# Optimization experiments

Measured on AMD Instinct MI355X. Metric: run time of the kernel, lower is better.

## Reference

```python
import jax, jax.numpy as jnp
import numpy as np
from math import sqrt

B, LQ, LKV = 4, 1024, 1024
QD = KD = VD = 1024
MODEL_DIM = 1024
H = 16
HD = MODEL_DIM // H  # per-head model_dim = 64


def setup_inputs() -> dict:
    key = jax.random.key(0)
    ks = jax.random.split(key, 10)
    s = 0.02
    return {
        "queries": jax.random.normal(ks[0], (B, LQ, QD), jnp.float32),
        "context": jax.random.normal(ks[1], (B, LKV, KD), jnp.float32),
        # stacked per-head linear weights (torch Linear: y = x @ W.T + b); store as [H, in, out]
        "Wq": jax.random.normal(ks[2], (H, QD, HD), jnp.float32) * s,
        "bq": jax.random.normal(ks[3], (H, HD), jnp.float32) * s,
        "Wk": jax.random.normal(ks[4], (KD, HD * 1 * H), jnp.float32).reshape(H, KD, HD) * s,
        "bk": jax.random.normal(ks[5], (H, HD), jnp.float32) * s,
        "Wv": jax.random.normal(ks[6], (H, VD, HD), jnp.float32) * s,
        "bv": jax.random.normal(ks[7], (H, HD), jnp.float32) * s,
        "Wo": jax.random.normal(ks[8], (H * HD, MODEL_DIM), jnp.float32) * s,
        "bo": jax.random.normal(ks[9], (MODEL_DIM,), jnp.float32) * s,
    }


def reference(queries, context, Wq, bq, Wk, bk, Wv, bv, Wo, bo):
    # queries: [B,Lq,Dq]; context: [B,Lkv,Dk]
    # Per-head projections, batched over heads (equivalent to the torch per-head loop).
    q = jnp.einsum("bld,hdm->bhlm", queries, Wq) + bq[None, :, None, :]  # [B,H,Lq,hd]
    k = jnp.einsum("bld,hdm->bhlm", context, Wk) + bk[None, :, None, :]  # [B,H,Lkv,hd]
    v = jnp.einsum("bld,hdm->bhlm", context, Wv) + bv[None, :, None, :]  # [B,H,Lkv,hd]

    scale = 1.0 / sqrt(HD)
    scores = jnp.einsum("bhqd,bhkd->bhqk", q, k) * scale  # [B,H,Lq,Lkv]
    att = jax.nn.softmax(scores, axis=-1)
    head_out = jnp.einsum("bhqk,bhkd->bhqd", att, v)  # [B,H,Lq,hd]

    # torch concatenates heads along the last dim in head order 0..H-1
    multi = head_out.transpose(0, 2, 1, 3).reshape(B, LQ, H * HD)
    residual = q.transpose(0, 2, 1, 3).reshape(B, LQ, H * HD)

    out = multi @ Wo + bo  # [B,Lq,model_dim]
    return out, residual
```

## Files before the change

kernel.cpp:

```cpp
#include <hip/hip_runtime.h>
#include <hip/hip_bf16.h>


typedef unsigned short u16;
typedef __attribute__((ext_vector_type(8))) short short8;
typedef __attribute__((ext_vector_type(4))) float f32x4;

__device__ __forceinline__ float bf2f(u16 u) {
    union { unsigned int i; float f; } c;
    c.i = ((unsigned int)u) << 16;
    return c.f;
}

__device__ __forceinline__ u16 f2bf(float f) {
    unsigned int x = __float_as_uint(f);
    unsigned int r = (x + 0x7fffu + ((x >> 16) & 1u)) >> 16;
    return (u16)r;
}

__device__ __forceinline__ void glds16(u16* lds, const u16* g) {
    __builtin_amdgcn_global_load_lds(
        (const __attribute__((address_space(1))) void*)g,
        (__attribute__((address_space(3))) void*)lds, 16, 0, 0);
}

__global__ __launch_bounds__(256) void prep(
    const float* __restrict__ q, const float* __restrict__ ctx,
    const float* __restrict__ Wq, const float* __restrict__ Wk,
    const float* __restrict__ Wv, const float* __restrict__ Wo,
    u16* __restrict__ Aq, u16* __restrict__ Ac,
    u16* __restrict__ Wqt, u16* __restrict__ Wkt,
    u16* __restrict__ Wvt, u16* __restrict__ Wot)
{
    __shared__ float ls[64][65];
    const int t = threadIdx.x;
    int bid = blockIdx.x;

    if (bid < 4096) {
        const float* in = (bid < 2048) ? q : ctx;
        u16* out = (bid < 2048) ? Aq : Ac;
        size_t i = ((size_t)(bid & 2047) * 256 + t) * 8;
        float4 v0 = *(const float4*)(in + i);
        float4 v1 = *(const float4*)(in + i + 4);
        short8 p;
        p[0] = (short)f2bf(v0.x); p[1] = (short)f2bf(v0.y);
        p[2] = (short)f2bf(v0.z); p[3] = (short)f2bf(v0.w);
        p[4] = (short)f2bf(v1.x); p[5] = (short)f2bf(v1.y);
        p[6] = (short)f2bf(v1.z); p[7] = (short)f2bf(v1.w);
        *(short8*)(out + i) = p;
        return;
    }
    bid -= 4096;
    const float* in; u16* out; int C; size_t moff; int rt, ct;
    if (bid < 768) {
        const int m = bid >> 8, idx = bid & 255;
        in = (m == 0) ? Wq : (m == 1) ? Wk : Wv;
        out = (m == 0) ? Wqt : (m == 1) ? Wkt : Wvt;
        C = 64; rt = (idx & 15) * 64; ct = 0; moff = (size_t)(idx >> 4) * 65536;
    } else {
        const int idx = bid - 768;
        in = Wo; out = Wot; C = 1024; moff = 0;
        rt = (idx & 15) * 64; ct = (idx >> 4) * 64;
    }
    #pragma unroll
    for (int i = 0; i < 4; ++i) {
        int s = i * 256 + t;
        int row = s >> 4, chunk = s & 15;
        float4 v = *(const float4*)(in + moff + (size_t)(rt + row) * C + ct + chunk * 4);
        ls[row][chunk * 4 + 0] = v.x;
        ls[row][chunk * 4 + 1] = v.y;
        ls[row][chunk * 4 + 2] = v.z;
        ls[row][chunk * 4 + 3] = v.w;
    }
    __syncthreads();
    #pragma unroll
    for (int i = 0; i < 2; ++i) {
        int s = i * 256 + t;
        int n = s >> 3, kc = s & 7;
        short8 p;
        #pragma unroll
        for (int j = 0; j < 8; ++j) p[j] = (short)f2bf(ls[kc * 8 + j][n]);
        *(short8*)(out + moff + (size_t)(ct + n) * 1024 + rt + kc * 8) = p;
    }
}

__device__ __forceinline__ void gemm_core(
    const u16* __restrict__ A, const u16* __restrict__ Wt,
    int m0, u16* As, u16* Bs, f32x4 (&acc)[4][4])
{
    const int t = threadIdx.x;
    const int w = t >> 6, lane = t & 63;
    const int quad = lane >> 4, c = lane & 15;
    const int srow = w * 32 + (lane >> 2);
    const int sch = lane & 3;

    const u16* gA = A + (size_t)(m0 + srow) * 1024 + sch * 8;
    const u16* gB = Wt + (size_t)srow * 1024 + sch * 8;
    u16* lA = As + w * 32 * 32;
    u16* lB = Bs + w * 32 * 32;
    const u16* afr = As + ((w >> 1) * 64 + c) * 32 + quad * 8;
    const u16* bfr = Bs + ((w & 1) * 64 + c) * 32 + quad * 8;

    for (int kt = 0; kt < 1024; kt += 32) {
        glds16(lA,           gA + kt);
        glds16(lA + 16 * 32, gA + kt + 16 * 1024);
        glds16(lB,           gB + kt);
        glds16(lB + 16 * 32, gB + kt + 16 * 1024);
        __syncthreads();
        short8 af[4], bf[4];
        #pragma unroll
        for (int rs = 0; rs < 4; ++rs) af[rs] = *(const short8*)(afr + rs * 16 * 32);
        #pragma unroll
        for (int cs = 0; cs < 4; ++cs) bf[cs] = *(const short8*)(bfr + cs * 16 * 32);
        #pragma unroll
        for (int rs = 0; rs < 4; ++rs)
            #pragma unroll
            for (int cs = 0; cs < 4; ++cs)
                acc[rs][cs] = __builtin_amdgcn_mfma_f32_16x16x32_bf16(
                    af[rs], bf[cs], acc[rs][cs], 0, 0, 0);
        __syncthreads();
    }
}

__global__ __launch_bounds__(256, 3) void gemm_qkv(
    const u16* __restrict__ Aq, const u16* __restrict__ Ac,
    const u16* __restrict__ Wqt, const u16* __restrict__ Wkt,
    const u16* __restrict__ Wvt,
    const float* __restrict__ bq, const float* __restrict__ bk,
    const float* __restrict__ bv,
    u16* __restrict__ qws, u16* __restrict__ kws, u16* __restrict__ vtws,
    float* __restrict__ resid)
{
    __shared__ u16 As[128 * 32];
    __shared__ u16 Bs[128 * 32];
    const int n0 = blockIdx.x * 128, m0 = blockIdx.y * 128, z = blockIdx.z;
    const int t = threadIdx.x;
    const int w = t >> 6, lane = t & 63;
    const int quad = lane >> 4, c = lane & 15;

    const u16* A = (z == 0) ? Aq : Ac;
    const u16* Wt = ((z == 0) ? Wqt : (z == 1) ? Wkt : Wvt) + (size_t)n0 * 1024;
    const float* bias = (z == 0) ? bq : (z == 1) ? bk : bv;

    f32x4 acc[4][4] = {};
    gemm_core(A, Wt, m0, As, Bs, acc);

    const int h = blockIdx.x * 2 + (w & 1);
    float bb[4];
    #pragma unroll
    for (int cs = 0; cs < 4; ++cs) bb[cs] = bias[h * 64 + cs * 16 + c];

    if (z == 2) {
        #pragma unroll
        for (int rs = 0; rs < 4; ++rs) {
            const int l0 = m0 + (w >> 1) * 64 + rs * 16 + quad * 4;
            const int b = l0 >> 10, l = l0 & 1023;
            #pragma unroll
            for (int cs = 0; cs < 4; ++cs) {
                const int hd = cs * 16 + c;
                ushort4 pk;
                pk.x = f2bf(acc[rs][cs][0] + bb[cs]);
                pk.y = f2bf(acc[rs][cs][1] + bb[cs]);
                pk.z = f2bf(acc[rs][cs][2] + bb[cs]);
                pk.w = f2bf(acc[rs][cs][3] + bb[cs]);
                *(ushort4*)(vtws + ((size_t)(b * 16 + h) * 64 + hd) * 1024 + l) = pk;
            }
        }
    } else {
        u16* dst = (z == 0) ? qws : kws;
        const float scale = (z == 0) ? 0.125f : 1.0f;
        #pragma unroll
        for (int rs = 0; rs < 4; ++rs) {
            #pragma unroll
            for (int r = 0; r < 4; ++r) {
                const int row = m0 + (w >> 1) * 64 + rs * 16 + quad * 4 + r;
                const int b = row >> 10, l = row & 1023;
                u16* drow = dst + (((size_t)(b * 16 + h) * 1024) + l) * 64;
                float* rrow = (z == 0) ? (resid + (size_t)row * 1024 + h * 64) : nullptr;
                #pragma unroll
                for (int cs = 0; cs < 4; ++cs) {
                    float v = acc[rs][cs][r] + bb[cs];
                    drow[cs * 16 + c] = f2bf(v * scale);
                    if (z == 0) rrow[cs * 16 + c] = v;
                }
            }
        }
    }
}

__global__ __launch_bounds__(256, 3) void gemm_out(
    const u16* __restrict__ A, const u16* __restrict__ Wot,
    const float* __restrict__ bo, float* __restrict__ out)
{
    __shared__ u16 As[128 * 32];
    __shared__ u16 Bs[64 * 32];
    const int f = blockIdx.x;
    const int xcd = f & 7, k = f >> 3;
    const int m0 = (xcd * 4 + (k & 3)) * 128;
    const int n0 = (k >> 2) * 64;
    const int t = threadIdx.x;
    const int w = t >> 6, lane = t & 63;
    const int quad = lane >> 4, c = lane & 15;

    const int arow = w * 32 + (lane >> 2), ach = lane & 3;
    const int brow = w * 16 + (lane >> 2);
    const u16* gA = A + (size_t)(m0 + arow) * 1024 + ach * 8;
    const u16* gB = Wot + (size_t)(n0 + brow) * 1024 + ach * 8;
    u16* lA = As + w * 32 * 32;
    u16* lB = Bs + w * 16 * 32;
    const u16* afr = As + ((w >> 1) * 64 + c) * 32 + quad * 8;
    const u16* bfr = Bs + ((w & 1) * 32 + c) * 32 + quad * 8;

    f32x4 acc[4][2] = {};
    for (int kt = 0; kt < 1024; kt += 32) {
        glds16(lA,           gA + kt);
        glds16(lA + 16 * 32, gA + kt + 16 * 1024);
        glds16(lB,           gB + kt);
        __syncthreads();
        short8 af[4], bf[2];
        #pragma unroll
        for (int rs = 0; rs < 4; ++rs) af[rs] = *(const short8*)(afr + rs * 16 * 32);
        #pragma unroll
        for (int cs = 0; cs < 2; ++cs) bf[cs] = *(const short8*)(bfr + cs * 16 * 32);
        #pragma unroll
        for (int rs = 0; rs < 4; ++rs)
            #pragma unroll
            for (int cs = 0; cs < 2; ++cs)
                acc[rs][cs] = __builtin_amdgcn_mfma_f32_16x16x32_bf16(
                    af[rs], bf[cs], acc[rs][cs], 0, 0, 0);
        __syncthreads();
    }

    const int nb = n0 + (w & 1) * 32;
    float bb[2];
    #pragma unroll
    for (int cs = 0; cs < 2; ++cs) bb[cs] = bo[nb + cs * 16 + c];

    #pragma unroll
    for (int rs = 0; rs < 4; ++rs) {
        #pragma unroll
        for (int r = 0; r < 4; ++r) {
            const int row = m0 + (w >> 1) * 64 + rs * 16 + quad * 4 + r;
            float* orow = out + (size_t)row * 1024 + nb;
            #pragma unroll
            for (int cs = 0; cs < 2; ++cs)
                orow[cs * 16 + c] = acc[rs][cs][r] + bb[cs];
        }
    }
}

__global__ __launch_bounds__(256, 4) void attn_mfma(
    const u16* __restrict__ qws, const u16* __restrict__ kws,
    const u16* __restrict__ vtws, u16* __restrict__ multi)
{
    __shared__ u16 Ks[64 * 64];
    __shared__ u16 Vs[64 * 64];
    const int t = threadIdx.x;
    const int wave = t >> 6, lane = t & 63;
    const int quad = lane >> 4, c = lane & 15;
    const int bh = blockIdx.y, b = bh >> 4, h = bh & 15;
    const int q0 = blockIdx.x * 64 + wave * 16;

    const u16* qb = qws + ((size_t)bh * 1024 + q0) * 64;
    const u16* kb = kws + (size_t)bh * 65536;
    const u16* vb = vtws + (size_t)bh * 65536;

    short8 qa0 = *(const short8*)(qb + (size_t)c * 64 + quad * 8);
    short8 qa1 = *(const short8*)(qb + (size_t)c * 64 + 32 + quad * 8);

    const int srow = wave * 16 + (lane >> 3);
    const int gch = (lane & 7) ^ ((lane >> 3) & 7);
    u16* ldsK0 = Ks + (wave * 16) * 64;
    u16* ldsK1 = Ks + (wave * 16 + 8) * 64;
    u16* ldsV0 = Vs + (wave * 16) * 64;
    u16* ldsV1 = Vs + (wave * 16 + 8) * 64;
    const u16* gK0 = kb + (size_t)srow * 64 + gch * 8;
    const u16* gK1 = kb + (size_t)(srow + 8) * 64 + gch * 8;
    const u16* gV0 = vb + (size_t)srow * 1024 + gch * 8;
    const u16* gV1 = vb + (size_t)(srow + 8) * 1024 + gch * 8;

    f32x4 O[4] = {};
    float lsum = 0.f;
    const int cx = c & 7;

    for (int kt = 0; kt < 1024; kt += 64) {
        glds16(ldsK0, gK0 + (size_t)kt * 64);
        glds16(ldsK1, gK1 + (size_t)kt * 64);
        glds16(ldsV0, gV0 + kt);
        glds16(ldsV1, gV1 + kt);
        __syncthreads();

        #pragma unroll
        for (int hb = 0; hb < 2; ++hb) {
            const int kbase = hb * 32;
            const u16* kr0 = Ks + (kbase + c) * 64;
            const u16* kr1 = Ks + (kbase + 16 + c) * 64;
            short8 kf00 = *(const short8*)(kr0 + (quad ^ cx) * 8);
            short8 kf01 = *(const short8*)(kr0 + ((4 + quad) ^ cx) * 8);
            short8 kf10 = *(const short8*)(kr1 + (quad ^ cx) * 8);
            short8 kf11 = *(const short8*)(kr1 + ((4 + quad) ^ cx) * 8);

            f32x4 st0 = {}, st1 = {};
            st0 = __builtin_amdgcn_mfma_f32_16x16x32_bf16(kf00, qa0, st0, 0, 0, 0);
            st0 = __builtin_amdgcn_mfma_f32_16x16x32_bf16(kf01, qa1, st0, 0, 0, 0);
            st1 = __builtin_amdgcn_mfma_f32_16x16x32_bf16(kf10, qa0, st1, 0, 0, 0);
            st1 = __builtin_amdgcn_mfma_f32_16x16x32_bf16(kf11, qa1, st1, 0, 0, 0);

            f32x4 p0, p1;
            #pragma unroll
            for (int r = 0; r < 4; ++r) {
                p0[r] = __expf(st0[r]);
                p1[r] = __expf(st1[r]);
                lsum += p0[r] + p1[r];
            }

            short8 pa;
            #pragma unroll
            for (int j = 0; j < 8; ++j) {
                const int srcl = ((2 * quad + (j >> 2)) & 3) * 16 + c;
                float v0 = __shfl(p0[j & 3], srcl);
                float v1 = __shfl(p1[j & 3], srcl);
                float v = (quad < 2) ? v0 : v1;
                pa[j] = (short)(__float_as_uint(v) >> 16);
            }

            #pragma unroll
            for (int nt = 0; nt < 4; ++nt) {
                const u16* vr = Vs + (nt * 16 + c) * 64;
                short8 vf = *(const short8*)(vr + ((hb * 4 + quad) ^ cx) * 8);
                O[nt] = __builtin_amdgcn_mfma_f32_16x16x32_bf16(pa, vf, O[nt], 0, 0, 0);
            }
        }
        __syncthreads();
    }

    lsum += __shfl_xor(lsum, 16);
    lsum += __shfl_xor(lsum, 32);
    float inv[4];
    #pragma unroll
    for (int r = 0; r < 4; ++r) inv[r] = 1.0f / __shfl(lsum, quad * 4 + r);

    u16* ob = multi + ((size_t)b * 1024 + q0 + quad * 4) * 1024 + h * 64 + c;
    #pragma unroll
    for (int r = 0; r < 4; ++r) {
        u16* orow = ob + (size_t)r * 1024;
        orow[0]  = f2bf(O[0][r] * inv[r]);
        orow[16] = f2bf(O[1][r] * inv[r]);
        orow[32] = f2bf(O[2][r] * inv[r]);
        orow[48] = f2bf(O[3][r] * inv[r]);
    }
}

extern "C" void kernel_launch(void* const* d_in, const int* in_sizes, int n_in,
                              void* d_out, int out_size, void* d_ws, size_t ws_size,
                              hipStream_t stream) {
    const float* queries = (const float*)d_in[0];
    const float* context = (const float*)d_in[1];
    const float* Wq = (const float*)d_in[2];
    const float* bq = (const float*)d_in[3];
    const float* Wk = (const float*)d_in[4];
    const float* bk = (const float*)d_in[5];
    const float* Wv = (const float*)d_in[6];
    const float* bv = (const float*)d_in[7];
    const float* Wo = (const float*)d_in[8];
    const float* bo = (const float*)d_in[9];

    float* out = (float*)d_out;
    float* resid = out + (size_t)4 * 1024 * 1024;

    const size_t M1 = 1024 * 1024;
    u16* Aq   = (u16*)d_ws;
    u16* Ac   = Aq + 4 * M1;
    u16* Wqt  = Ac + 4 * M1;
    u16* Wkt  = Wqt + M1;
    u16* Wvt  = Wkt + M1;
    u16* Wot  = Wvt + M1;
    u16* qws  = Wot + M1;
    u16* kws  = qws + 4 * M1;
    u16* vtws = kws + 4 * M1;
    u16* mws  = vtws + 4 * M1;

    prep<<<5120, 256, 0, stream>>>(queries, context, Wq, Wk, Wv, Wo,
                                   Aq, Ac, Wqt, Wkt, Wvt, Wot);
    gemm_qkv<<<dim3(8, 32, 3), 256, 0, stream>>>(Aq, Ac, Wqt, Wkt, Wvt,
                                                 bq, bk, bv, qws, kws, vtws, resid);
    attn_mfma<<<dim3(16, 64), 256, 0, stream>>>(qws, kws, vtws, mws);
    gemm_out<<<512, 256, 0, stream>>>(mws, Wot, bo, out);
}
```

Before: 212.0 us.

## Fuse K and V projections sharing context tiles; route attention P through LDS

The QKV projection kernel now computes K and V in the same block, so each context tile is loaded into LDS once and multiplied against both weight tiles. This halves context-tile traffic for the K/V GEMMs but doubles accumulator registers, lowers the occupancy bound to 2 and leaves z=0 blocks doing half the work of z=1 blocks (load imbalance). The attention kernel switches from shuffle-based transposition of P to writing P as bf16 into a per-wave padded LDS buffer and reading it back as the A operand. Row sums are reduced with xor-shuffles across the 16 columns.

```diff
diff --git a/kernel.cpp b/kernel.cpp
--- a/kernel.cpp
+++ b/kernel.cpp
@@ -84,45 +84,7 @@
     }
 }
 
-__device__ __forceinline__ void gemm_core(
-    const u16* __restrict__ A, const u16* __restrict__ Wt,
-    int m0, u16* As, u16* Bs, f32x4 (&acc)[4][4])
-{
-    const int t = threadIdx.x;
-    const int w = t >> 6, lane = t & 63;
-    const int quad = lane >> 4, c = lane & 15;
-    const int srow = w * 32 + (lane >> 2);
-    const int sch = lane & 3;
-
-    const u16* gA = A + (size_t)(m0 + srow) * 1024 + sch * 8;
-    const u16* gB = Wt + (size_t)srow * 1024 + sch * 8;
-    u16* lA = As + w * 32 * 32;
-    u16* lB = Bs + w * 32 * 32;
-    const u16* afr = As + ((w >> 1) * 64 + c) * 32 + quad * 8;
-    const u16* bfr = Bs + ((w & 1) * 64 + c) * 32 + quad * 8;
-
-    for (int kt = 0; kt < 1024; kt += 32) {
-        glds16(lA,           gA + kt);
-        glds16(lA + 16 * 32, gA + kt + 16 * 1024);
-        glds16(lB,           gB + kt);
-        glds16(lB + 16 * 32, gB + kt + 16 * 1024);
-        __syncthreads();
-        short8 af[4], bf[4];
-        #pragma unroll
-        for (int rs = 0; rs < 4; ++rs) af[rs] = *(const short8*)(afr + rs * 16 * 32);
-        #pragma unroll
-        for (int cs = 0; cs < 4; ++cs) bf[cs] = *(const short8*)(bfr + cs * 16 * 32);
-        #pragma unroll
-        for (int rs = 0; rs < 4; ++rs)
-            #pragma unroll
-            for (int cs = 0; cs < 4; ++cs)
-                acc[rs][cs] = __builtin_amdgcn_mfma_f32_16x16x32_bf16(
-                    af[rs], bf[cs], acc[rs][cs], 0, 0, 0);
-        __syncthreads();
-    }
-}
-
-__global__ __launch_bounds__(256, 3) void gemm_qkv(
+__global__ __launch_bounds__(256, 2) void gemm_qkv(
     const u16* __restrict__ Aq, const u16* __restrict__ Ac,
     const u16* __restrict__ Wqt, const u16* __restrict__ Wkt,
     const u16* __restrict__ Wvt,
@@ -132,57 +94,125 @@
     float* __restrict__ resid)
 {
     __shared__ u16 As[128 * 32];
-    __shared__ u16 Bs[128 * 32];
+    __shared__ u16 B1[128 * 32];
+    __shared__ u16 B2[128 * 32];
     const int n0 = blockIdx.x * 128, m0 = blockIdx.y * 128, z = blockIdx.z;
     const int t = threadIdx.x;
     const int w = t >> 6, lane = t & 63;
     const int quad = lane >> 4, c = lane & 15;
-
-    const u16* A = (z == 0) ? Aq : Ac;
-    const u16* Wt = ((z == 0) ? Wqt : (z == 1) ? Wkt : Wvt) + (size_t)n0 * 1024;
-    const float* bias = (z == 0) ? bq : (z == 1) ? bk : bv;
-
-    f32x4 acc[4][4] = {};
-    gemm_core(A, Wt, m0, As, Bs, acc);
-
+    const int srow = w * 32 + (lane >> 2);
+    const int sch = lane & 3;
+
+    u16* lA = As + w * 32 * 32;
+    u16* lB1 = B1 + w * 32 * 32;
+    u16* lB2 = B2 + w * 32 * 32;
+    const u16* afr = As + ((w >> 1) * 64 + c) * 32 + quad * 8;
+    const u16* b1fr = B1 + ((w & 1) * 64 + c) * 32 + quad * 8;
+    const u16* b2fr = B2 + ((w & 1) * 64 + c) * 32 + quad * 8;
     const int h = blockIdx.x * 2 + (w & 1);
-    float bb[4];
-    #pragma unroll
-    for (int cs = 0; cs < 4; ++cs) bb[cs] = bias[h * 64 + cs * 16 + c];
-
-    if (z == 2) {
+
+    if (z == 0) {
+        const u16* gA = Aq + (size_t)(m0 + srow) * 1024 + sch * 8;
+        const u16* gB = Wqt + (size_t)(n0 + srow) * 1024 + sch * 8;
+        f32x4 acc[4][4] = {};
+        for (int kt = 0; kt < 1024; kt += 32) {
+            glds16(lA,           gA + kt);
+            glds16(lA + 16 * 32, gA + kt + 16 * 1024);
+            glds16(lB1,           gB + kt);
+            glds16(lB1 + 16 * 32, gB + kt + 16 * 1024);
+            __syncthreads();
+            short8 af[4], bf[4];
+            #pragma unroll
+            for (int rs = 0; rs < 4; ++rs) af[rs] = *(const short8*)(afr + rs * 16 * 32);
+            #pragma unroll
+            for (int cs = 0; cs < 4; ++cs) bf[cs] = *(const short8*)(b1fr + cs * 16 * 32);
+            #pragma unroll
+            for (int rs = 0; rs < 4; ++rs)
+                #pragma unroll
+                for (int cs = 0; cs < 4; ++cs)
+                    acc[rs][cs] = __builtin_amdgcn_mfma_f32_16x16x32_bf16(
+                        af[rs], bf[cs], acc[rs][cs], 0, 0, 0);
+            __syncthreads();
+        }
+        float bb[4];
+        #pragma unroll
+        for (int cs = 0; cs < 4; ++cs) bb[cs] = bq[h * 64 + cs * 16 + c];
+        #pragma unroll
+        for (int rs = 0; rs < 4; ++rs)
+            #pragma unroll
+            for (int r = 0; r < 4; ++r) {
+                const int row = m0 + (w >> 1) * 64 + rs * 16 + quad * 4 + r;
+                const int b = row >> 10, l = row & 1023;
+                u16* drow = qws + (((size_t)(b * 16 + h) * 1024) + l) * 64;
+                float* rrow = resid + (size_t)row * 1024 + h * 64;
+                #pragma unroll
+                for (int cs = 0; cs < 4; ++cs) {
+                    float v = acc[rs][cs][r] + bb[cs];
+                    drow[cs * 16 + c] = f2bf(v * 0.125f);
+                    rrow[cs * 16 + c] = v;
+                }
+            }
+    } else {
+        const u16* gA = Ac + (size_t)(m0 + srow) * 1024 + sch * 8;
+        const u16* gBk = Wkt + (size_t)(n0 + srow) * 1024 + sch * 8;
+        const u16* gBv = Wvt + (size_t)(n0 + srow) * 1024 + sch * 8;
+        f32x4 acck[4][4] = {};
+        f32x4 accv[4][4] = {};
+        for (int kt = 0; kt < 1024; kt += 32) {
+            glds16(lA,            gA + kt);
+            glds16(lA + 16 * 32,  gA + kt + 16 * 1024);
+            glds16(lB1,           gBk + kt);
+            glds16(lB1 + 16 * 32, gBk + kt + 16 * 1024);
+            glds16(lB2,           gBv + kt);
+            glds16(lB2 + 16 * 32, gBv + kt + 16 * 1024);
+            __syncthreads();
+            short8 af[4], bkf[4], bvf[4];
+            #pragma unroll
+            for (int rs = 0; rs < 4; ++rs) af[rs] = *(const short8*)(afr + rs * 16 * 32);
+            #pragma unroll
+            for (int cs = 0; cs < 4; ++cs) {
+                bkf[cs] = *(const short8*)(b1fr + cs * 16 * 32);
+                bvf[cs] = *(const short8*)(b2fr + cs * 16 * 32);
+            }
+            #pragma unroll
+            for (int rs = 0; rs < 4; ++rs)
+                #pragma unroll
+                for (int cs = 0; cs < 4; ++cs) {
+                    acck[rs][cs] = __builtin_amdgcn_mfma_f32_16x16x32_bf16(
+                        af[rs], bkf[cs], acck[rs][cs], 0, 0, 0);
+                    accv[rs][cs] = __builtin_amdgcn_mfma_f32_16x16x32_bf16(
+                        af[rs], bvf[cs], accv[rs][cs], 0, 0, 0);
+                }
+            __syncthreads();
+        }
+        float bbk[4], bbv[4];
+        #pragma unroll
+        for (int cs = 0; cs < 4; ++cs) {
+            bbk[cs] = bk[h * 64 + cs * 16 + c];
+            bbv[cs] = bv[h * 64 + cs * 16 + c];
+        }
         #pragma unroll
         for (int rs = 0; rs < 4; ++rs) {
+            #pragma unroll
+            for (int r = 0; r < 4; ++r) {
+                const int row = m0 + (w >> 1) * 64 + rs * 16 + quad * 4 + r;
+                const int b = row >> 10, l = row & 1023;
+                u16* drow = kws + (((size_t)(b * 16 + h) * 1024) + l) * 64;
+                #pragma unroll
+                for (int cs = 0; cs < 4; ++cs)
+                    drow[cs * 16 + c] = f2bf(acck[rs][cs][r] + bbk[cs]);
+            }
             const int l0 = m0 + (w >> 1) * 64 + rs * 16 + quad * 4;
             const int b = l0 >> 10, l = l0 & 1023;
             #pragma unroll
             for (int cs = 0; cs < 4; ++cs) {
                 const int hd = cs * 16 + c;
                 ushort4 pk;
-                pk.x = f2bf(acc[rs][cs][0] + bb[cs]);
-                pk.y = f2bf(acc[rs][cs][1] + bb[cs]);
-                pk.z = f2bf(acc[rs][cs][2] + bb[cs]);
-                pk.w = f2bf(acc[rs][cs][3] + bb[cs]);
+                pk.x = f2bf(accv[rs][cs][0] + bbv[cs]);
+                pk.y = f2bf(accv[rs][cs][1] + bbv[cs]);
+                pk.z = f2bf(accv[rs][cs][2] + bbv[cs]);
+                pk.w = f2bf(accv[rs][cs][3] + bbv[cs]);
                 *(ushort4*)(vtws + ((size_t)(b * 16 + h) * 64 + hd) * 1024 + l) = pk;
-            }
-        }
-    } else {
-        u16* dst = (z == 0) ? qws : kws;
-        const float scale = (z == 0) ? 0.125f : 1.0f;
-        #pragma unroll
-        for (int rs = 0; rs < 4; ++rs) {
-            #pragma unroll
-            for (int r = 0; r < 4; ++r) {
-                const int row = m0 + (w >> 1) * 64 + rs * 16 + quad * 4 + r;
-                const int b = row >> 10, l = row & 1023;
-                u16* drow = dst + (((size_t)(b * 16 + h) * 1024) + l) * 64;
-                float* rrow = (z == 0) ? (resid + (size_t)row * 1024 + h * 64) : nullptr;
-                #pragma unroll
-                for (int cs = 0; cs < 4; ++cs) {
-                    float v = acc[rs][cs][r] + bb[cs];
-                    drow[cs * 16 + c] = f2bf(v * scale);
-                    if (z == 0) rrow[cs * 16 + c] = v;
-                }
             }
         }
     }
@@ -255,6 +285,7 @@
 {
     __shared__ u16 Ks[64 * 64];
     __shared__ u16 Vs[64 * 64];
+    __shared__ u16 Ps[4][16 * 72];
     const int t = threadIdx.x;
     const int wave = t >> 6, lane = t & 63;
     const int quad = lane >> 4, c = lane & 15;
@@ -280,7 +311,8 @@
     const u16* gV1 = vb + (size_t)(srow + 8) * 1024 + gch * 8;
 
     f32x4 O[4] = {};
-    float lsum = 0.f;
+    float ps[4] = {0.f, 0.f, 0.f, 0.f};
+    u16* pw = &Ps[wave][0];
     const int cx = c & 7;
 
     for (int kt = 0; kt < 1024; kt += 64) {
@@ -290,55 +322,50 @@
         glds16(ldsV1, gV1 + kt);
         __syncthreads();
 
-        #pragma unroll
-        for (int hb = 0; hb < 2; ++hb) {
-            const int kbase = hb * 32;
-            const u16* kr0 = Ks + (kbase + c) * 64;
-            const u16* kr1 = Ks + (kbase + 16 + c) * 64;
-            short8 kf00 = *(const short8*)(kr0 + (quad ^ cx) * 8);
-            short8 kf01 = *(const short8*)(kr0 + ((4 + quad) ^ cx) * 8);
-            short8 kf10 = *(const short8*)(kr1 + (quad ^ cx) * 8);
-            short8 kf11 = *(const short8*)(kr1 + ((4 + quad) ^ cx) * 8);
-
-            f32x4 st0 = {}, st1 = {};
-            st0 = __builtin_amdgcn_mfma_f32_16x16x32_bf16(kf00, qa0, st0, 0, 0, 0);
-            st0 = __builtin_amdgcn_mfma_f32_16x16x32_bf16(kf01, qa1, st0, 0, 0, 0);
-            st1 = __builtin_amdgcn_mfma_f32_16x16x32_bf16(kf10, qa0, st1, 0, 0, 0);
-            st1 = __builtin_amdgcn_mfma_f32_16x16x32_bf16(kf11, qa1, st1, 0, 0, 0);
-
-            f32x4 p0, p1;
+        f32x4 s[4];
+        #pragma unroll
+        for (int nt = 0; nt < 4; ++nt) {
+            const u16* kr = Ks + (nt * 16 + c) * 64;
+            short8 kb0 = *(const short8*)(kr + ((quad ^ cx)) * 8);
+            short8 kb1 = *(const short8*)(kr + (((4 + quad) ^ cx)) * 8);
+            f32x4 z = {};
+            z = __builtin_amdgcn_mfma_f32_16x16x32_bf16(qa0, kb0, z, 0, 0, 0);
+            z = __builtin_amdgcn_mfma_f32_16x16x32_bf16(qa1, kb1, z, 0, 0, 0);
+            s[nt] = z;
+        }
+
+        #pragma unroll
+        for (int nt = 0; nt < 4; ++nt)
             #pragma unroll
             for (int r = 0; r < 4; ++r) {
-                p0[r] = __expf(st0[r]);
-                p1[r] = __expf(st1[r]);
-                lsum += p0[r] + p1[r];
+                float p = __expf(s[nt][r]);
+                ps[r] += p;
+                pw[(quad * 4 + r) * 72 + nt * 16 + c] = (u16)(__float_as_uint(p) >> 16);
             }
-
-            short8 pa;
-            #pragma unroll
-            for (int j = 0; j < 8; ++j) {
-                const int srcl = ((2 * quad + (j >> 2)) & 3) * 16 + c;
-                float v0 = __shfl(p0[j & 3], srcl);
-                float v1 = __shfl(p1[j & 3], srcl);
-                float v = (quad < 2) ? v0 : v1;
-                pa[j] = (short)(__float_as_uint(v) >> 16);
-            }
-
-            #pragma unroll
-            for (int nt = 0; nt < 4; ++nt) {
-                const u16* vr = Vs + (nt * 16 + c) * 64;
-                short8 vf = *(const short8*)(vr + ((hb * 4 + quad) ^ cx) * 8);
-                O[nt] = __builtin_amdgcn_mfma_f32_16x16x32_bf16(pa, vf, O[nt], 0, 0, 0);
-            }
+        short8 pa0 = *(const short8*)(pw + c * 72 + quad * 8);
+        short8 pa1 = *(const short8*)(pw + c * 72 + 32 + quad * 8);
+
+        #pragma unroll
+        for (int nt = 0; nt < 4; ++nt) {
+            const u16* vr = Vs + (nt * 16 + c) * 64;
+            short8 vb0 = *(const short8*)(vr + ((quad ^ cx)) * 8);
+            short8 vb1 = *(const short8*)(vr + (((4 + quad) ^ cx)) * 8);
+            O[nt] = __builtin_amdgcn_mfma_f32_16x16x32_bf16(pa0, vb0, O[nt], 0, 0, 0);
+            O[nt] = __builtin_amdgcn_mfma_f32_16x16x32_bf16(pa1, vb1, O[nt], 0, 0, 0);
         }
         __syncthreads();
     }
 
-    lsum += __shfl_xor(lsum, 16);
-    lsum += __shfl_xor(lsum, 32);
     float inv[4];
     #pragma unroll
-    for (int r = 0; r < 4; ++r) inv[r] = 1.0f / __shfl(lsum, quad * 4 + r);
+    for (int r = 0; r < 4; ++r) {
+        float sum = ps[r];
+        sum += __shfl_xor(sum, 1);
+        sum += __shfl_xor(sum, 2);
+        sum += __shfl_xor(sum, 4);
+        sum += __shfl_xor(sum, 8);
+        inv[r] = 1.0f / sum;
+    }
 
     u16* ob = multi + ((size_t)b * 1024 + q0 + quad * 4) * 1024 + h * 64 + c;
     #pragma unroll
@@ -382,7 +409,7 @@
 
     prep<<<5120, 256, 0, stream>>>(queries, context, Wq, Wk, Wv, Wo,
                                    Aq, Ac, Wqt, Wkt, Wvt, Wot);
-    gemm_qkv<<<dim3(8, 32, 3), 256, 0, stream>>>(Aq, Ac, Wqt, Wkt, Wvt,
+    gemm_qkv<<<dim3(8, 32, 2), 256, 0, stream>>>(Aq, Ac, Wqt, Wkt, Wvt,
                                                  bq, bk, bv, qws, kws, vtws, resid);
     attn_mfma<<<dim3(16, 64), 256, 0, stream>>>(qws, kws, vtws, mws);
     gemm_out<<<512, 256, 0, stream>>>(mws, Wot, bo, out);
```

Result: faster. 202.1 us (-4.7%).

## Split attention KV range across waves with cross-wave reduction and XCD-aware block mapping

Applied to the files above, without the earlier changes.

Restructures the attention kernel so every wave processes all 64 queries of the block over its own quarter of the KV sequence, staging K/V per wave without block barriers, then reduces partial outputs and row sums across waves through LDS. Probabilities go through per-wave LDS instead of lane shuffles, and blocks are remapped so each XCD handles a contiguous set of batch-heads for L2 reuse. The aim is to remove per-tile __syncthreads and shuffle overhead and to raise MFMA reuse of each K/V fragment. In exchange it uses more LDS and registers (occupancy hint lowered to 2), and partial outputs are rounded to bf16 before the cross-wave sum, which adds rounding error.

```diff
diff --git a/kernel.cpp b/kernel.cpp
--- a/kernel.cpp
+++ b/kernel.cpp
@@ -3,18 +3,19 @@
 
 
 typedef unsigned short u16;
+typedef unsigned int u32;
 typedef __attribute__((ext_vector_type(8))) short short8;
 typedef __attribute__((ext_vector_type(4))) float f32x4;
 
 __device__ __forceinline__ float bf2f(u16 u) {
-    union { unsigned int i; float f; } c;
-    c.i = ((unsigned int)u) << 16;
-    return c.f;
+    union { u32 i; float f; } cv;
+    cv.i = ((u32)u) << 16;
+    return cv.f;
 }
 
 __device__ __forceinline__ u16 f2bf(float f) {
-    unsigned int x = __float_as_uint(f);
-    unsigned int r = (x + 0x7fffu + ((x >> 16) & 1u)) >> 16;
+    u32 x = __float_as_uint(f);
+    u32 r = (x + 0x7fffu + ((x >> 16) & 1u)) >> 16;
     return (u16)r;
 }
 
@@ -249,105 +250,163 @@
     }
 }
 
-__global__ __launch_bounds__(256, 4) void attn_mfma(
+__global__ __launch_bounds__(256, 2) void attn_mfma(
     const u16* __restrict__ qws, const u16* __restrict__ kws,
     const u16* __restrict__ vtws, u16* __restrict__ multi)
 {
-    __shared__ u16 Ks[64 * 64];
-    __shared__ u16 Vs[64 * 64];
+    __shared__ u16 smem[26112];
     const int t = threadIdx.x;
-    const int wave = t >> 6, lane = t & 63;
+    const int w = t >> 6, lane = t & 63;
     const int quad = lane >> 4, c = lane & 15;
-    const int bh = blockIdx.y, b = bh >> 4, h = bh & 15;
-    const int q0 = blockIdx.x * 64 + wave * 16;
+    const int f = blockIdx.x;
+    const int xcd = f & 7, j = f >> 3;
+    const int bh = xcd * 8 + (j & 7);
+    const int qt = j >> 3;
+    const int b = bh >> 4, h = bh & 15;
+    const int q0 = qt * 64;
 
     const u16* qb = qws + ((size_t)bh * 1024 + q0) * 64;
     const u16* kb = kws + (size_t)bh * 65536;
     const u16* vb = vtws + (size_t)bh * 65536;
 
-    short8 qa0 = *(const short8*)(qb + (size_t)c * 64 + quad * 8);
-    short8 qa1 = *(const short8*)(qb + (size_t)c * 64 + 32 + quad * 8);
-
-    const int srow = wave * 16 + (lane >> 3);
-    const int gch = (lane & 7) ^ ((lane >> 3) & 7);
-    u16* ldsK0 = Ks + (wave * 16) * 64;
-    u16* ldsK1 = Ks + (wave * 16 + 8) * 64;
-    u16* ldsV0 = Vs + (wave * 16) * 64;
-    u16* ldsV1 = Vs + (wave * 16 + 8) * 64;
-    const u16* gK0 = kb + (size_t)srow * 64 + gch * 8;
-    const u16* gK1 = kb + (size_t)(srow + 8) * 64 + gch * 8;
-    const u16* gV0 = vb + (size_t)srow * 1024 + gch * 8;
-    const u16* gV1 = vb + (size_t)(srow + 8) * 1024 + gch * 8;
-
-    f32x4 O[4] = {};
-    float lsum = 0.f;
+    short8 qa[4][2];
+    #pragma unroll
+    for (int mt = 0; mt < 4; ++mt) {
+        const u16* qr = qb + (size_t)(mt * 16 + c) * 64 + quad * 8;
+        qa[mt][0] = *(const short8*)(qr);
+        qa[mt][1] = *(const short8*)(qr + 32);
+    }
+
+    u16* stgK = smem + w * 4096;
+    u16* stgV = stgK + 2048;
+    u16* pw   = smem + 16384 + w * 2304;
+    float* lsumLDS = (float*)(smem + 25600);
+
+    const int gkc = (lane & 7) ^ ((lane >> 3) & 7);
+    const int gvc = (lane & 3) ^ ((lane >> 3) & 3);
+    const int krow = lane >> 3;
+    const int vdim = lane >> 2;
+
+    f32x4 O[4][4] = {};
+    f32x4 lp[4] = {};
+    const int kw = w * 256;
     const int cx = c & 7;
-
-    for (int kt = 0; kt < 1024; kt += 64) {
-        glds16(ldsK0, gK0 + (size_t)kt * 64);
-        glds16(ldsK1, gK1 + (size_t)kt * 64);
-        glds16(ldsV0, gV0 + kt);
-        glds16(ldsV1, gV1 + kt);
-        __syncthreads();
-
-        #pragma unroll
-        for (int hb = 0; hb < 2; ++hb) {
-            const int kbase = hb * 32;
-            const u16* kr0 = Ks + (kbase + c) * 64;
-            const u16* kr1 = Ks + (kbase + 16 + c) * 64;
-            short8 kf00 = *(const short8*)(kr0 + (quad ^ cx) * 8);
-            short8 kf01 = *(const short8*)(kr0 + ((4 + quad) ^ cx) * 8);
-            short8 kf10 = *(const short8*)(kr1 + (quad ^ cx) * 8);
-            short8 kf11 = *(const short8*)(kr1 + ((4 + quad) ^ cx) * 8);
-
-            f32x4 st0 = {}, st1 = {};
-            st0 = __builtin_amdgcn_mfma_f32_16x16x32_bf16(kf00, qa0, st0, 0, 0, 0);
-            st0 = __builtin_amdgcn_mfma_f32_16x16x32_bf16(kf01, qa1, st0, 0, 0, 0);
-            st1 = __builtin_amdgcn_mfma_f32_16x16x32_bf16(kf10, qa0, st1, 0, 0, 0);
-            st1 = __builtin_amdgcn_mfma_f32_16x16x32_bf16(kf11, qa1, st1, 0, 0, 0);
-
-            f32x4 p0, p1;
+    const int vsw = quad ^ ((c >> 1) & 3);
+
+    for (int i = 0; i < 8; ++i) {
+        const int kt = kw + i * 32;
+        #pragma unroll
+        for (int jj = 0; jj < 4; ++jj)
+            glds16(stgK + jj * 512, kb + (size_t)(kt + jj * 8 + krow) * 64 + gkc * 8);
+        #pragma unroll
+        for (int jj = 0; jj < 4; ++jj)
+            glds16(stgV + jj * 512, vb + (size_t)(jj * 16 + vdim) * 1024 + kt + gvc * 8);
+        __asm__ volatile("s_waitcnt vmcnt(0)" ::: "memory");
+
+        short8 kf[2][2];
+        #pragma unroll
+        for (int nt = 0; nt < 2; ++nt)
+            #pragma unroll
+            for (int kh = 0; kh < 2; ++kh)
+                kf[nt][kh] = *(const short8*)(stgK + (nt * 16 + c) * 64
+                                              + (((kh * 4 + quad)) ^ cx) * 8);
+
+        #pragma unroll
+        for (int mt = 0; mt < 4; ++mt) {
+            f32x4 s0 = {}, s1 = {};
+            s0 = __builtin_amdgcn_mfma_f32_16x16x32_bf16(qa[mt][0], kf[0][0], s0, 0, 0, 0);
+            s0 = __builtin_amdgcn_mfma_f32_16x16x32_bf16(qa[mt][1], kf[0][1], s0, 0, 0, 0);
+            s1 = __builtin_amdgcn_mfma_f32_16x16x32_bf16(qa[mt][0], kf[1][0], s1, 0, 0, 0);
+            s1 = __builtin_amdgcn_mfma_f32_16x16x32_bf16(qa[mt][1], kf[1][1], s1, 0, 0, 0);
             #pragma unroll
             for (int r = 0; r < 4; ++r) {
-                p0[r] = __expf(st0[r]);
-                p1[r] = __expf(st1[r]);
-                lsum += p0[r] + p1[r];
+                float p0 = __expf(s0[r]);
+                float p1 = __expf(s1[r]);
+                lp[mt][r] += p0 + p1;
+                const int prow = (mt * 16 + quad * 4 + r) * 36;
+                pw[prow + c]      = (u16)(__float_as_uint(p0) >> 16);
+                pw[prow + 16 + c] = (u16)(__float_as_uint(p1) >> 16);
             }
-
-            short8 pa;
-            #pragma unroll
-            for (int j = 0; j < 8; ++j) {
-                const int srcl = ((2 * quad + (j >> 2)) & 3) * 16 + c;
-                float v0 = __shfl(p0[j & 3], srcl);
-                float v1 = __shfl(p1[j & 3], srcl);
-                float v = (quad < 2) ? v0 : v1;
-                pa[j] = (short)(__float_as_uint(v) >> 16);
-            }
-
-            #pragma unroll
-            for (int nt = 0; nt < 4; ++nt) {
-                const u16* vr = Vs + (nt * 16 + c) * 64;
-                short8 vf = *(const short8*)(vr + ((hb * 4 + quad) ^ cx) * 8);
-                O[nt] = __builtin_amdgcn_mfma_f32_16x16x32_bf16(pa, vf, O[nt], 0, 0, 0);
-            }
-        }
-        __syncthreads();
-    }
-
-    lsum += __shfl_xor(lsum, 16);
-    lsum += __shfl_xor(lsum, 32);
-    float inv[4];
-    #pragma unroll
-    for (int r = 0; r < 4; ++r) inv[r] = 1.0f / __shfl(lsum, quad * 4 + r);
-
-    u16* ob = multi + ((size_t)b * 1024 + q0 + quad * 4) * 1024 + h * 64 + c;
+        }
+
+        short8 vf[4];
+        #pragma unroll
+        for (int nt = 0; nt < 4; ++nt)
+            vf[nt] = *(const short8*)(stgV + (nt * 16 + c) * 32 + vsw * 8);
+        #pragma unroll
+        for (int mt = 0; mt < 4; ++mt) {
+            short8 pa = *(const short8*)(pw + (mt * 16 + c) * 36 + quad * 8);
+            #pragma unroll
+            for (int nt = 0; nt < 4; ++nt)
+                O[mt][nt] = __builtin_amdgcn_mfma_f32_16x16x32_bf16(
+                    pa, vf[nt], O[mt][nt], 0, 0, 0);
+        }
+        __asm__ volatile("s_waitcnt lgkmcnt(0)" ::: "memory");
+    }
+
+    __syncthreads();
+
+    #pragma unroll
+    for (int mt = 0; mt < 4; ++mt)
+        #pragma unroll
+        for (int r = 0; r < 4; ++r) {
+            float v = lp[mt][r];
+            v += __shfl_xor(v, 1);
+            v += __shfl_xor(v, 2);
+            v += __shfl_xor(v, 4);
+            v += __shfl_xor(v, 8);
+            lp[mt][r] = v;
+        }
+    if (c < 4) {
+        #pragma unroll
+        for (int mt = 0; mt < 4; ++mt)
+            lsumLDS[w * 64 + mt * 16 + quad * 4 + c] = lp[mt][c];
+    }
+
+    u32* ex = (u32*)smem;
+    #pragma unroll
+    for (int mt = 0; mt < 4; ++mt)
+        #pragma unroll
+        for (int nt = 0; nt < 4; ++nt) {
+            u32 lo = (u32)f2bf(O[mt][nt][0]) | ((u32)f2bf(O[mt][nt][1]) << 16);
+            u32 hi = (u32)f2bf(O[mt][nt][2]) | ((u32)f2bf(O[mt][nt][3]) << 16);
+            uint2 pk; pk.x = lo; pk.y = hi;
+            *(uint2*)(ex + w * 2048 + (mt * 4 + nt) * 128 + lane * 2) = pk;
+        }
+    __syncthreads();
+
+    float ls[4];
+    #pragma unroll
+    for (int r = 0; r < 4; ++r) {
+        float s = 0.f;
+        #pragma unroll
+        for (int wp = 0; wp < 4; ++wp)
+            s += lsumLDS[wp * 64 + w * 16 + quad * 4 + r];
+        ls[r] = 1.0f / s;
+    }
+
+    float fo[4][4];
+    #pragma unroll
+    for (int nt = 0; nt < 4; ++nt) {
+        float a0 = 0.f, a1 = 0.f, a2 = 0.f, a3 = 0.f;
+        #pragma unroll
+        for (int wp = 0; wp < 4; ++wp) {
+            uint2 pk = *(const uint2*)(ex + wp * 2048 + (w * 4 + nt) * 128 + lane * 2);
+            a0 += bf2f((u16)(pk.x & 0xffff));
+            a1 += bf2f((u16)(pk.x >> 16));
+            a2 += bf2f((u16)(pk.y & 0xffff));
+            a3 += bf2f((u16)(pk.y >> 16));
+        }
+        fo[nt][0] = a0; fo[nt][1] = a1; fo[nt][2] = a2; fo[nt][3] = a3;
+    }
+
+    u16* ob = multi + ((size_t)b * 1024 + q0 + w * 16 + quad * 4) * 1024 + h * 64 + c;
     #pragma unroll
     for (int r = 0; r < 4; ++r) {
         u16* orow = ob + (size_t)r * 1024;
-        orow[0]  = f2bf(O[0][r] * inv[r]);
-        orow[16] = f2bf(O[1][r] * inv[r]);
-        orow[32] = f2bf(O[2][r] * inv[r]);
-        orow[48] = f2bf(O[3][r] * inv[r]);
+        #pragma unroll
+        for (int nt = 0; nt < 4; ++nt)
+            orow[nt * 16] = f2bf(fo[nt][r] * ls[r]);
     }
 }
 
@@ -384,6 +443,6 @@
                                    Aq, Ac, Wqt, Wkt, Wvt, Wot);
     gemm_qkv<<<dim3(8, 32, 3), 256, 0, stream>>>(Aq, Ac, Wqt, Wkt, Wvt,
                                                  bq, bk, bv, qws, kws, vtws, resid);
-    attn_mfma<<<dim3(16, 64), 256, 0, stream>>>(qws, kws, vtws, mws);
+    attn_mfma<<<1024, 256, 0, stream>>>(qws, kws, vtws, mws);
     gemm_out<<<512, 256, 0, stream>>>(mws, Wot, bo, out);
 }
```

New measurement: 204.2 us. 1.04x faster.
